# Kernel tuning notes

Hardware: AMD Instinct MI355X
Metric: run time of the kernel (lower is better)

## Reference

```python
import jax, jax.numpy as jnp
import numpy as np

EPS = 1e-12  # undefined global `eps` in the original source; standard tiny epsilon


def setup_inputs() -> dict:
    key = jax.random.key(0)
    k1, k2 = jax.random.split(key)
    B, C = 32768, 1000
    output = jax.random.normal(k1, (B, C), dtype=jnp.float32)
    multilabels = (jax.random.uniform(k2, (B, C)) < 0.05).astype(jnp.float32)
    multilabels = multilabels.at[:, 0].set(1.0)
    return {"output": output, "multilabels": multilabels}


def reference(output, multilabels):
    # Equivalent closed form of: for every nonempty subset g of true labels,
    #   loss(g) = -[ pseudo_y*log(o+eps) + (1-pseudo_y)*log(1-o+eps) ].sum()
    #           = base - sum_{j in g} gain_j,
    # with base = -sum_j log(1-o_j+eps) and gain_j = log(o_j+eps)-log(1-o_j+eps).
    # min over nonempty subsets = base - max nonempty-subset gain
    #   = base - (sum of positive gains over true labels, or the max single
    #      gain among true labels if all gains are negative).
    o = jax.nn.sigmoid(output)                      # [B, C]
    log_p = jnp.log(o + EPS)
    log_np = jnp.log(1.0 - o + EPS)
    base = -jnp.sum(log_np, axis=1)                 # [B]
    gain = log_p - log_np                           # [B, C]
    is_true = multilabels == 1.0                    # [B, C] bool (constant)
    pos = is_true & (gain > 0)
    pos_gain = jnp.sum(jnp.where(pos, gain, 0.0), axis=1)          # [B]
    any_pos = jnp.any(pos, axis=1)                                  # [B]
    best_single = jnp.max(jnp.where(is_true, gain, -jnp.inf), axis=1)  # [B]
    max_gain = jnp.where(any_pos, pos_gain, best_single)
    per_sample = base - max_gain                    # [B]
    return jnp.mean(per_sample)
```

## Files before the change

### kernel.cpp

```cpp
#include <hip/hip_runtime.h>
#include <math.h>

#define EPS 1e-12f

constexpr int B = 32768;
constexpr int C = 1000;
constexpr int C4 = C / 4;
constexpr int BLOCKS = 2048;
constexpr int THREADS = 256;
constexpr int WAVES_PER_BLOCK = THREADS / 64;
constexpr int TOTAL_WAVES = BLOCKS * WAVES_PER_BLOCK;

__device__ __forceinline__ void elem_update(float x, float m,
                                            float& base, float& pos, float& best) {
    float o  = 1.0f / (1.0f + __expf(-x));
    float lp = __logf(o + EPS);
    float ln = __logf(1.0f - o + EPS);
    base -= ln;
    float g = lp - ln;
    if (m == 1.0f) {
        if (g > 0.0f) pos += g;
        best = fmaxf(best, g);
    }
}

__global__ __launch_bounds__(THREADS)
void row_loss_kernel(const float* __restrict__ out_logits,
                     const float* __restrict__ labels,
                     float* __restrict__ partial) {
    const int wave_in_block = threadIdx.x >> 6;
    const int lane          = threadIdx.x & 63;
    const int gwave         = blockIdx.x * WAVES_PER_BLOCK + wave_in_block;

    float acc = 0.0f;

    for (int row = gwave; row < B; row += TOTAL_WAVES) {
        const float4* o4 = reinterpret_cast<const float4*>(out_logits + (size_t)row * C);
        const float4* m4 = reinterpret_cast<const float4*>(labels     + (size_t)row * C);

        float base = 0.0f, pos = 0.0f, best = -INFINITY;

        for (int k = lane; k < C4; k += 64) {
            float4 x = o4[k];
            float4 m = m4[k];
            elem_update(x.x, m.x, base, pos, best);
            elem_update(x.y, m.y, base, pos, best);
            elem_update(x.z, m.z, base, pos, best);
            elem_update(x.w, m.w, base, pos, best);
        }

        #pragma unroll
        for (int off = 32; off > 0; off >>= 1) {
            base += __shfl_down(base, off, 64);
            pos  += __shfl_down(pos,  off, 64);
            best  = fmaxf(best, __shfl_down(best, off, 64));
        }

        if (lane == 0) {
            float max_gain = (pos > 0.0f) ? pos : best;
            acc += base - max_gain;
        }
    }

    __shared__ float s[WAVES_PER_BLOCK];
    if (lane == 0) s[wave_in_block] = acc;
    __syncthreads();
    if (threadIdx.x == 0) {
        float t = 0.0f;
        #pragma unroll
        for (int i = 0; i < WAVES_PER_BLOCK; ++i) t += s[i];
        partial[blockIdx.x] = t;
    }
}

__global__ __launch_bounds__(256)
void finalize_kernel(const float* __restrict__ partial, float* __restrict__ out) {
    double t = 0.0;
    for (int i = threadIdx.x; i < BLOCKS; i += 256) t += (double)partial[i];

    #pragma unroll
    for (int off = 32; off > 0; off >>= 1)
        t += __shfl_down(t, off, 64);

    __shared__ double s[4];
    const int lane = threadIdx.x & 63;
    const int w    = threadIdx.x >> 6;
    if (lane == 0) s[w] = t;
    __syncthreads();
    if (threadIdx.x == 0) {
        double r = s[0] + s[1] + s[2] + s[3];
        out[0] = (float)(r / (double)B);
    }
}

extern "C" void kernel_launch(void* const* d_in, const int* in_sizes, int n_in,
                              void* d_out, int out_size, void* d_ws, size_t ws_size,
                              hipStream_t stream) {
    const float* out_logits = (const float*)d_in[0];
    const float* labels     = (const float*)d_in[1];
    float* out              = (float*)d_out;
    float* partial          = (float*)d_ws;

    row_loss_kernel<<<BLOCKS, THREADS, 0, stream>>>(out_logits, labels, partial);
    finalize_kernel<<<1, 256, 0, stream>>>(partial, out);
}
```

Measured before the change: 279.0 us.

## Use softplus closed form for the loss and hoist all row loads up front

Rewrites the per-element math with the identities gain = x and -log(1-sigmoid(x)) = softplus(x), so each element needs one exp and one log instead of a reciprocal, an exp and two logs. The column loop is fully unrolled into four float4 loads per input issued before any compute, with four independent accumulator sets, so more memory requests are in flight. The tail lanes are padded with -inf logits and zero labels. Dropping EPS and the sigmoid saturation slightly changes numerics for large |x|.

```diff
diff --git a/kernel.cpp b/kernel.cpp
--- a/kernel.cpp
+++ b/kernel.cpp
@@ -1,7 +1,6 @@
 #include <hip/hip_runtime.h>
 #include <math.h>
 
-#define EPS 1e-12f
 
 constexpr int B = 32768;
 constexpr int C = 1000;
@@ -10,23 +9,28 @@
 constexpr int THREADS = 256;
 constexpr int WAVES_PER_BLOCK = THREADS / 64;
 constexpr int TOTAL_WAVES = BLOCKS * WAVES_PER_BLOCK;
+constexpr int TAIL_LANES = C4 - 192;
 
 __device__ __forceinline__ void elem_update(float x, float m,
                                             float& base, float& pos, float& best) {
-    float o  = 1.0f / (1.0f + __expf(-x));
-    float lp = __logf(o + EPS);
-    float ln = __logf(1.0f - o + EPS);
-    base -= ln;
-    float g = lp - ln;
-    if (m == 1.0f) {
-        if (g > 0.0f) pos += g;
-        best = fmaxf(best, g);
-    }
+    float e  = __expf(-fabsf(x));
+    float xp = fmaxf(x, 0.0f);
+    base += xp + __logf(1.0f + e);
+    pos  += m * xp;
+    if (m != 0.0f) best = fmaxf(best, x);
+}
+
+__device__ __forceinline__ void vec_update(float4 x, float4 m,
+                                           float& base, float& pos, float& best) {
+    elem_update(x.x, m.x, base, pos, best);
+    elem_update(x.y, m.y, base, pos, best);
+    elem_update(x.z, m.z, base, pos, best);
+    elem_update(x.w, m.w, base, pos, best);
 }
 
 __global__ __launch_bounds__(THREADS)
-void row_loss_kernel(const float* __restrict__ out_logits,
-                     const float* __restrict__ labels,
+void row_loss_kernel(const float* __restrict__ X,
+                     const float* __restrict__ M,
                      float* __restrict__ partial) {
     const int wave_in_block = threadIdx.x >> 6;
     const int lane          = threadIdx.x & 63;
@@ -35,19 +39,34 @@
     float acc = 0.0f;
 
     for (int row = gwave; row < B; row += TOTAL_WAVES) {
-        const float4* o4 = reinterpret_cast<const float4*>(out_logits + (size_t)row * C);
-        const float4* m4 = reinterpret_cast<const float4*>(labels     + (size_t)row * C);
+        const float4* x4 = reinterpret_cast<const float4*>(X + (size_t)row * C);
+        const float4* m4 = reinterpret_cast<const float4*>(M + (size_t)row * C);
 
-        float base = 0.0f, pos = 0.0f, best = -INFINITY;
+        float4 xa = x4[lane];
+        float4 xb = x4[lane + 64];
+        float4 xc = x4[lane + 128];
+        float4 ma = m4[lane];
+        float4 mb = m4[lane + 64];
+        float4 mc = m4[lane + 128];
+        float4 xd = make_float4(-INFINITY, -INFINITY, -INFINITY, -INFINITY);
+        float4 md = make_float4(0.0f, 0.0f, 0.0f, 0.0f);
+        if (lane < TAIL_LANES) {
+            xd = x4[lane + 192];
+            md = m4[lane + 192];
+        }
 
-        for (int k = lane; k < C4; k += 64) {
-            float4 x = o4[k];
-            float4 m = m4[k];
-            elem_update(x.x, m.x, base, pos, best);
-            elem_update(x.y, m.y, base, pos, best);
-            elem_update(x.z, m.z, base, pos, best);
-            elem_update(x.w, m.w, base, pos, best);
-        }
+        float b0 = 0.f, b1 = 0.f, b2 = 0.f, b3 = 0.f;
+        float p0 = 0.f, p1 = 0.f, p2 = 0.f, p3 = 0.f;
+        float s0 = -INFINITY, s1 = -INFINITY, s2 = -INFINITY, s3 = -INFINITY;
+
+        vec_update(xa, ma, b0, p0, s0);
+        vec_update(xb, mb, b1, p1, s1);
+        vec_update(xc, mc, b2, p2, s2);
+        vec_update(xd, md, b3, p3, s3);
+
+        float base = (b0 + b1) + (b2 + b3);
+        float pos  = (p0 + p1) + (p2 + p3);
+        float best = fmaxf(fmaxf(s0, s1), fmaxf(s2, s3));
 
         #pragma unroll
         for (int off = 32; off > 0; off >>= 1) {
@@ -96,11 +115,11 @@
 extern "C" void kernel_launch(void* const* d_in, const int* in_sizes, int n_in,
                               void* d_out, int out_size, void* d_ws, size_t ws_size,
                               hipStream_t stream) {
-    const float* out_logits = (const float*)d_in[0];
-    const float* labels     = (const float*)d_in[1];
-    float* out              = (float*)d_out;
-    float* partial          = (float*)d_ws;
+    const float* X   = (const float*)d_in[0];
+    const float* M   = (const float*)d_in[1];
+    float* out       = (float*)d_out;
+    float* partial   = (float*)d_ws;
 
-    row_loss_kernel<<<BLOCKS, THREADS, 0, stream>>>(out_logits, labels, partial);
+    row_loss_kernel<<<BLOCKS, THREADS, 0, stream>>>(X, M, partial);
     finalize_kernel<<<1, 256, 0, stream>>>(partial, out);
 }
```

Measured after the change: 271.8 us. 1.03x faster.
